# Kernel tuning notes

Measured on AMD Instinct MI355X. Metric: run time of the kernel, lower is better.

## Reference

```python
import jax, jax.numpy as jnp
import numpy as np

N = 50000   # nodes
E = 400000  # edges
H = 4       # heads
C = 64      # hidden per head
IN = 8
G = 64      # graphs in batch
NEG_SLOPE = 0.2


def setup_inputs() -> dict:
    key = jax.random.key(0)
    ks = jax.random.split(key, 32)
    def w(k, shape, fan_in):
        return jax.random.normal(k, shape, jnp.float32) * (1.0 / np.sqrt(fan_in))
    inp = {}
    inp['x'] = jax.random.normal(ks[0], (N, IN), jnp.float32)
    inp['edge_index'] = jax.random.randint(ks[1], (2, E), 0, N, jnp.int32)
    inp['edge_attr'] = jax.random.normal(ks[2], (E, 1), jnp.float32)
    inp['batch'] = jnp.sort(jax.random.randint(ks[3], (N,), 0, G, jnp.int32))
    # encoder
    inp['enc_w'] = w(ks[4], (IN, H * 16), IN)[:, :64]  # [8,64]
    inp['enc_b'] = jnp.zeros((64,), jnp.float32)
    # gat1: in 64 -> H*C = 256
    inp['g1_wl'] = w(ks[5], (64, H * C), 64)
    inp['g1_bl'] = jnp.zeros((H * C,), jnp.float32)
    inp['g1_wr'] = w(ks[6], (64, H * C), 64)
    inp['g1_we'] = w(ks[7], (1, H * C), 1)
    inp['g1_att'] = w(ks[8], (H, C), C)
    inp['g1_b'] = jnp.zeros((H * C,), jnp.float32)
    # gat2: in 256 -> H*C = 256
    inp['g2_wl'] = w(ks[9], (H * C, H * C), H * C)
    inp['g2_bl'] = jnp.zeros((H * C,), jnp.float32)
    inp['g2_wr'] = w(ks[10], (H * C, H * C), H * C)
    inp['g2_we'] = w(ks[11], (1, H * C), 1)
    inp['g2_att'] = w(ks[12], (H, C), C)
    inp['g2_b'] = jnp.zeros((H * C,), jnp.float32)
    # post MLP: 256 -> 128 -> LN -> ReLU -> 128 -> 64 -> ReLU
    inp['p1_w'] = w(ks[13], (H * C, 128), H * C)
    inp['p1_b'] = jnp.zeros((128,), jnp.float32)
    inp['ln_g'] = jnp.ones((128,), jnp.float32)
    inp['ln_b'] = jnp.zeros((128,), jnp.float32)
    inp['p2_w'] = w(ks[14], (128, 64), 128)
    inp['p2_b'] = jnp.zeros((64,), jnp.float32)
    inp['head_w'] = w(ks[15], (64, 1), 64)
    inp['head_b'] = jnp.zeros((1,), jnp.float32)
    return inp


def gatv2_conv(h, src, dst, ea, wl, bl, wr, we, att, b):
    # PyG GATv2Conv (concat=True): message from src j aggregated at dst i
    xl = (h @ wl + bl).reshape(N, H, C)   # lin_l(x_j), carries source messages
    xr = (h @ wr).reshape(N, H, C)        # lin_r(x_i)
    e = (ea @ we).reshape(E, H, C)        # lin_edge(edge_attr)
    s = jax.nn.leaky_relu(xl[src] + xr[dst] + e, NEG_SLOPE)  # [E,H,C]
    logits = jnp.einsum('ehc,hc->eh', s, att)                # [E,H]
    # softmax over incoming edges of each dst node
    mx = jax.ops.segment_max(logits, dst, num_segments=N)
    ex = jnp.exp(logits - mx[dst])
    denom = jax.ops.segment_sum(ex, dst, num_segments=N)
    alpha = ex / (denom[dst] + 1e-16)                        # [E,H]
    out = jax.ops.segment_sum(alpha[:, :, None] * xl[src], dst, num_segments=N)
    return out.reshape(N, H * C) + b


def reference(x, edge_index, edge_attr, batch, enc_w, enc_b,
              g1_wl, g1_bl, g1_wr, g1_we, g1_att, g1_b,
              g2_wl, g2_bl, g2_wr, g2_we, g2_att, g2_b,
              p1_w, p1_b, ln_g, ln_b, p2_w, p2_b, head_w, head_b):
    src, dst = edge_index[0], edge_index[1]
    h = jax.nn.relu(x @ enc_w + enc_b)
    h = jax.nn.relu(gatv2_conv(h, src, dst, edge_attr, g1_wl, g1_bl, g1_wr, g1_we, g1_att, g1_b))
    h = jax.nn.relu(gatv2_conv(h, src, dst, edge_attr, g2_wl, g2_bl, g2_wr, g2_we, g2_att, g2_b))
    # global mean pool per graph
    s = jax.ops.segment_sum(h, batch, num_segments=G)
    cnt = jax.ops.segment_sum(jnp.ones((N,), h.dtype), batch, num_segments=G)
    g = s / jnp.maximum(cnt, 1.0)[:, None]                   # [G, H*C]
    # post MLP (dropout is identity in eval)
    z = g @ p1_w + p1_b
    mu = jnp.mean(z, axis=-1, keepdims=True)
    var = jnp.mean((z - mu) ** 2, axis=-1, keepdims=True)
    z = (z - mu) * jax.lax.rsqrt(var + 1e-5) * ln_g + ln_b
    z = jax.nn.relu(z)
    z = jax.nn.relu(z @ p2_w + p2_b)
    return (z @ head_w + head_b).squeeze(-1)                 # [G]
```

## Files before the change

kernel.cpp:

```cpp
#include <hip/hip_runtime.h>
#include <hip/hip_bf16.h>
#include <math.h>

#define NN 50000
#define NE 400000
#define HH 4
#define CC 64
#define HC 256
#define GG 64
#define NB 196
#define ENCB 12500
#define WCB 640

typedef short v8s __attribute__((ext_vector_type(8)));
typedef float f32x4 __attribute__((ext_vector_type(4)));

static __device__ inline unsigned short f2bf(float v) {
  __hip_bfloat16 b = __float2bfloat16(v);
  return *reinterpret_cast<unsigned short*>(&b);
}
static __device__ inline float bflo(unsigned u) { return __uint_as_float(u << 16); }
static __device__ inline float bfhi(unsigned u) { return __uint_as_float(u & 0xffff0000u); }

static __device__ inline void gload_lds16(const void* g, void* l) {
  __builtin_amdgcn_global_load_lds(
      (const __attribute__((address_space(1))) void*)g,
      (__attribute__((address_space(3))) void*)l, 16, 0, 0);
}

__global__ __launch_bounds__(256) void head_kernel(
    const float* __restrict__ x, const float* __restrict__ enc_w,
    const float* __restrict__ enc_b, unsigned short* __restrict__ h0,
    const float* __restrict__ g1_wl, const float* __restrict__ g1_wr,
    const float* __restrict__ g2_wl, const float* __restrict__ g2_wr,
    unsigned short* __restrict__ wt1, unsigned short* __restrict__ wt2,
    const int* __restrict__ batch, int* __restrict__ deg,
    float* __restrict__ pool, int* __restrict__ bounds) {
  int bid = blockIdx.x, tid = threadIdx.x;
  if (bid < ENCB) {
    int idx = bid * 256 + tid;
    int node = idx >> 6, col = idx & 63;
    const float* xr = x + node * 8;
    float acc = enc_b[col];
#pragma unroll
    for (int k = 0; k < 8; ++k) acc += xr[k] * enc_w[k * 64 + col];
    h0[idx] = f2bf(fmaxf(acc, 0.f));
  } else if (bid < ENCB + WCB) {
    int idx = (bid - ENCB) * 256 + tid;
    const float* W; unsigned short* Wt; int K; int base;
    if (idx < 16384)        { W = g1_wl; Wt = wt1;                     K = 64;  base = idx; }
    else if (idx < 32768)   { W = g1_wr; Wt = wt1 + (size_t)256 * 64;  K = 64;  base = idx - 16384; }
    else if (idx < 98304)   { W = g2_wl; Wt = wt2;                     K = 256; base = idx - 32768; }
    else if (idx < 163840)  { W = g2_wr; Wt = wt2 + (size_t)256 * 256; K = 256; base = idx - 98304; }
    else return;
    int k = base >> 8, n = base & 255;
    Wt[n * K + k] = f2bf(W[base]);
  } else {
    int sb = bid - ENCB - WCB;
    int i = sb * 256 + tid;
    if (i < NN) deg[i] = 0;
    if (sb < GG) pool[sb * 256 + tid] = 0.f;
    if (sb == NB - 1 && tid <= GG) {
      int g = tid, lo = 0, hi = NN;
      while (lo < hi) {
        int mid = (lo + hi) >> 1;
        if (batch[mid] < g) lo = mid + 1; else hi = mid;
      }
      bounds[g] = lo;
    }
  }
}

template <int K, bool FILL>
__global__ __launch_bounds__(256) void matmul_mfma_kernel(
    const unsigned short* __restrict__ A, const unsigned short* __restrict__ Wt,
    const float* __restrict__ bias,
    unsigned short* __restrict__ outL, unsigned short* __restrict__ outR, int M,
    const int* __restrict__ ei, const float* __restrict__ ea,
    int* __restrict__ cursor, int2* __restrict__ edges) {
  const int mmb = ((M + 127) >> 7) << 2;
  int bid = blockIdx.x;
  if (FILL && bid >= mmb) {
    int e = (bid - mmb) * 256 + threadIdx.x;
    if (e < NE) {
      int d = ei[NE + e];
      int pos = atomicAdd(&cursor[d], 1);
      edges[pos] = make_int2(ei[e] << 9, __float_as_int(ea[e]));
    }
    return;
  }
  {
    int q = mmb >> 3, r = mmb & 7;
    int xcd = bid & 7, off2 = bid >> 3;
    bid = (xcd < r ? xcd * (q + 1) : r * (q + 1) + (xcd - r) * q) + off2;
  }
  __shared__ __attribute__((aligned(16))) unsigned short lds[8192];
  const int tid = threadIdx.x;
  const int wave = tid >> 6;
  const int lane = tid & 63;
  const int quad = lane >> 4;
  const int lrow = lane & 15;
  const int wr = (wave & 1) * 64;
  const int wc = (wave >> 1) * 64;
  const int r0 = (bid >> 2) * 128;
  const int n0 = (bid & 3) * 128;

  f32x4 acc[4][4];
#pragma unroll
  for (int i = 0; i < 4; ++i)
#pragma unroll
    for (int j = 0; j < 4; ++j) acc[i][j] = (f32x4){0.f, 0.f, 0.f, 0.f};

  const int lrA0 = (wave * 2) * 16 + (lane >> 2);
  const int lrA1 = lrA0 + 16;
  const int c    = lane & 3;
  const int cs0  = c ^ ((lrA0 >> 1) & 3);
  const int cs1  = c ^ ((lrA1 >> 1) & 3);
  int ga0 = r0 + lrA0; if (ga0 >= M) ga0 = M - 1;
  int ga1 = r0 + lrA1; if (ga1 >= M) ga1 = M - 1;
  const unsigned short* srcA0 = A  + (size_t)ga0 * K + cs0 * 8;
  const unsigned short* srcA1 = A  + (size_t)ga1 * K + cs1 * 8;
  const unsigned short* srcB0 = Wt + (size_t)(n0 + lrA0) * K + cs0 * 8;
  const unsigned short* srcB1 = Wt + (size_t)(n0 + lrA1) * K + cs1 * 8;
  unsigned short* dA0 = &lds[(wave * 2 + 0) * 512];
  unsigned short* dA1 = &lds[(wave * 2 + 1) * 512];
  unsigned short* dB0 = &lds[4096 + (wave * 2 + 0) * 512];
  unsigned short* dB1 = &lds[4096 + (wave * 2 + 1) * 512];
  const int qsw = (quad ^ ((lrow >> 1) & 3)) * 8;

  for (int k0 = 0; k0 < K; k0 += 32) {
    gload_lds16(srcA0 + k0, dA0);
    gload_lds16(srcA1 + k0, dA1);
    gload_lds16(srcB0 + k0, dB0);
    gload_lds16(srcB1 + k0, dB1);
    __syncthreads();

    v8s af[4], bf[4];
#pragma unroll
    for (int rt = 0; rt < 4; ++rt)
      af[rt] = *(const v8s*)&lds[(wr + rt * 16 + lrow) * 32 + qsw];
#pragma unroll
    for (int ct = 0; ct < 4; ++ct)
      bf[ct] = *(const v8s*)&lds[4096 + (wc + ct * 16 + lrow) * 32 + qsw];
#pragma unroll
    for (int rt = 0; rt < 4; ++rt)
#pragma unroll
      for (int ct = 0; ct < 4; ++ct)
        acc[rt][ct] = __builtin_amdgcn_mfma_f32_16x16x32_bf16(af[rt], bf[ct], acc[rt][ct], 0, 0, 0);
    __syncthreads();
  }

  const bool isL = (n0 < 256);
  unsigned short* outp = isL ? outL : outR;
  const int cbase = isL ? n0 : (n0 - 256);
  constexpr int SP = 136;
  unsigned short* stage = lds;

#pragma unroll
  for (int rt = 0; rt < 4; ++rt) {
    __syncthreads();
#pragma unroll
    for (int ct = 0; ct < 4; ++ct) {
      int col = wc + ct * 16 + lrow;
      float b = isL ? bias[cbase + col] : 0.f;
#pragma unroll
      for (int r = 0; r < 4; ++r) {
        int sr = (wave & 1) * 16 + quad * 4 + r;
        stage[sr * SP + col] = f2bf(acc[rt][ct][r] + b);
      }
    }
    __syncthreads();
    int sr = tid >> 3;
    int c0 = (tid & 7) * 16;
    int grow = r0 + (sr >> 4) * 64 + rt * 16 + (sr & 15);
    if (grow < M) {
      uint4 v0 = *(const uint4*)&stage[sr * SP + c0];
      uint4 v1 = *(const uint4*)&stage[sr * SP + c0 + 8];
      *(uint4*)&outp[(size_t)grow * 256 + cbase + c0] = v0;
      *(uint4*)&outp[(size_t)grow * 256 + cbase + c0 + 8] = v1;
    }
  }
}

__global__ void degree_kernel(const int* __restrict__ ei, int* __restrict__ deg) {
  int e = blockIdx.x * 256 + threadIdx.x;
  if (e < NE) atomicAdd(&deg[ei[NE + e]], 1);
}

__global__ __launch_bounds__(256) void blocksum_kernel(
    const int* __restrict__ deg, int* __restrict__ bsum) {
  int t = threadIdx.x;
  int i = blockIdx.x * 256 + t;
  int v = (i < NN) ? deg[i] : 0;
#pragma unroll
  for (int off = 32; off; off >>= 1) v += __shfl_down(v, off, 64);
  __shared__ int ws[4];
  if ((t & 63) == 0) ws[t >> 6] = v;
  __syncthreads();
  if (t == 0) bsum[blockIdx.x] = ws[0] + ws[1] + ws[2] + ws[3];
}

__global__ __launch_bounds__(256) void blockscan_kernel(
    const int* __restrict__ bsum, int* __restrict__ bpre, int* __restrict__ rowstart) {
  __shared__ int s[256];
  int t = threadIdx.x;
  int v = (t < NB) ? bsum[t] : 0;
  s[t] = v;
  __syncthreads();
  for (int off = 1; off < 256; off <<= 1) {
    int x = s[t];
    int y = (t >= off) ? s[t - off] : 0;
    __syncthreads();
    s[t] = x + y;
    __syncthreads();
  }
  if (t < NB) bpre[t] = s[t] - v;
  if (t == 255) rowstart[NN] = s[255];
}

__global__ __launch_bounds__(256) void rowstart_kernel(
    const int* __restrict__ deg, const int* __restrict__ bpre,
    int* __restrict__ rowstart, int* __restrict__ cursor) {
  __shared__ int s[256];
  int t = threadIdx.x;
  int i = blockIdx.x * 256 + t;
  int v = (i < NN) ? deg[i] : 0;
  s[t] = v;
  __syncthreads();
  for (int off = 1; off < 256; off <<= 1) {
    int x = s[t];
    int y = (t >= off) ? s[t - off] : 0;
    __syncthreads();
    s[t] = x + y;
    __syncthreads();
  }
  if (i < NN) {
    int rs = bpre[blockIdx.x] + s[t] - v;
    rowstart[i] = rs;
    cursor[i] = rs;
  }
}

__global__ __launch_bounds__(256) void gat_fused_kernel(
    const int* __restrict__ rowstart, const int2* __restrict__ edges,
    const unsigned short* __restrict__ xl, const unsigned short* __restrict__ xr,
    const float* __restrict__ we, const float* __restrict__ att,
    const float* __restrict__ bias, unsigned short* __restrict__ outb) {
  int node = (blockIdx.x * 256 + threadIdx.x) >> 6;
  int lane = threadIdx.x & 63;
  int r0 = __builtin_amdgcn_readfirstlane(rowstart[node]);
  int r1 = __builtin_amdgcn_readfirstlane(rowstart[node + 1]);
  const char* xlp = (const char*)xl + lane * 8;
  uint2 rp = ((const uint2*)xr)[(size_t)node * 64 + lane];
  float4 r = make_float4(bflo(rp.x), bfhi(rp.x), bflo(rp.y), bfhi(rp.y));
  float4 wv = ((const float4*)we)[lane];
  float4 at = ((const float4*)att)[lane];
  const float LOG2E = 1.442695040888963f;
  at.x *= LOG2E; at.y *= LOG2E; at.z *= LOG2E; at.w *= LOG2E;
  float4 acc = make_float4(0.f, 0.f, 0.f, 0.f);
  float denom = 0.f;

  auto edge_step = [&](float eav, uint2 p) {
    float4 a = make_float4(bflo(p.x), bfhi(p.x), bflo(p.y), bfhi(p.y));
    float s0 = a.x + (r.x + eav * wv.x);
    float s1 = a.y + (r.y + eav * wv.y);
    float s2 = a.z + (r.z + eav * wv.z);
    float s3 = a.w + (r.w + eav * wv.w);
    s0 = fmaxf(s0, 0.2f * s0);
    s1 = fmaxf(s1, 0.2f * s1);
    s2 = fmaxf(s2, 0.2f * s2);
    s3 = fmaxf(s3, 0.2f * s3);
    float p4 = (s0 * at.x + s1 * at.y) + (s2 * at.z + s3 * at.w);
#pragma unroll
    for (int off = 8; off; off >>= 1) p4 += __shfl_xor(p4, off, 16);
    float ex = exp2f(p4);
    denom += ex;
    acc.x += ex * a.x; acc.y += ex * a.y; acc.z += ex * a.z; acc.w += ex * a.w;
  };

  int i = r0;
  for (; i + 4 <= r1; i += 4) {
    int2 e0 = edges[i];     int2 e1 = edges[i + 1];
    int2 e2 = edges[i + 2]; int2 e3 = edges[i + 3];
    uint2 p0 = *(const uint2*)(xlp + (unsigned)e0.x);
    uint2 p1 = *(const uint2*)(xlp + (unsigned)e1.x);
    uint2 p2 = *(const uint2*)(xlp + (unsigned)e2.x);
    uint2 p3 = *(const uint2*)(xlp + (unsigned)e3.x);
    edge_step(__int_as_float(e0.y), p0);
    edge_step(__int_as_float(e1.y), p1);
    edge_step(__int_as_float(e2.y), p2);
    edge_step(__int_as_float(e3.y), p3);
  }
  for (; i < r1; ++i) {
    int2 e = edges[i];
    edge_step(__int_as_float(e.y), *(const uint2*)(xlp + (unsigned)e.x));
  }

  float inv = 1.f / (denom + 1e-16f);
  float4 bv = ((const float4*)bias)[lane];
  float4 o;
  o.x = fmaxf(acc.x * inv + bv.x, 0.f);
  o.y = fmaxf(acc.y * inv + bv.y, 0.f);
  o.z = fmaxf(acc.z * inv + bv.z, 0.f);
  o.w = fmaxf(acc.w * inv + bv.w, 0.f);
  uint2 pk;
  pk.x = (unsigned)f2bf(o.x) | ((unsigned)f2bf(o.y) << 16);
  pk.y = (unsigned)f2bf(o.z) | ((unsigned)f2bf(o.w) << 16);
  ((uint2*)outb)[(size_t)node * 64 + lane] = pk;
}

__global__ __launch_bounds__(256) void pool_kernel(
    const unsigned short* __restrict__ h, const int* __restrict__ batch,
    float* __restrict__ pool) {
  int rg = threadIdx.x >> 6;
  int lane = threadIdx.x & 63;
  int n0 = blockIdx.x * 64;
  const uint2* h2 = (const uint2*)h;
  float4 acc = make_float4(0.f, 0.f, 0.f, 0.f);
  int cur = -1;
#pragma unroll 4
  for (int i = 0; i < 16; ++i) {
    int n = n0 + rg + 4 * i;
    if (n >= NN) break;
    int b = batch[n];
    if (b != cur) {
      if (cur >= 0) {
        float* p = &pool[cur * 256 + lane * 4];
        atomicAdd(p + 0, acc.x); atomicAdd(p + 1, acc.y);
        atomicAdd(p + 2, acc.z); atomicAdd(p + 3, acc.w);
      }
      cur = b;
      acc = make_float4(0.f, 0.f, 0.f, 0.f);
    }
    uint2 v = h2[(size_t)n * 64 + lane];
    acc.x += bflo(v.x); acc.y += bfhi(v.x);
    acc.z += bflo(v.y); acc.w += bfhi(v.y);
  }
  if (cur >= 0) {
    float* p = &pool[cur * 256 + lane * 4];
    atomicAdd(p + 0, acc.x); atomicAdd(p + 1, acc.y);
    atomicAdd(p + 2, acc.z); atomicAdd(p + 3, acc.w);
  }
}

__global__ __launch_bounds__(128) void mlp_kernel(
    const float* __restrict__ pool, const int* __restrict__ bounds,
    const float* __restrict__ p1w, const float* __restrict__ p1b,
    const float* __restrict__ lng, const float* __restrict__ lnb,
    const float* __restrict__ p2w, const float* __restrict__ p2b,
    const float* __restrict__ hw, const float* __restrict__ hb,
    float* __restrict__ out) {
  __shared__ float sg[256];
  __shared__ float red[128];
  __shared__ float sz[128];
  __shared__ float s2[64];
  int b = blockIdx.x, tid = threadIdx.x;
  float cntf = (float)(bounds[b + 1] - bounds[b]);
  float invc = 1.f / fmaxf(cntf, 1.f);
  for (int i = tid; i < 256; i += 128) sg[i] = pool[b * 256 + i] * invc;
  __syncthreads();
  float z = p1b[tid];
  for (int k = 0; k < 256; ++k) z += sg[k] * p1w[k * 128 + tid];
  red[tid] = z; __syncthreads();
  for (int off = 64; off; off >>= 1) { if (tid < off) red[tid] += red[tid + off]; __syncthreads(); }
  float mu = red[0] * (1.f / 128.f);
  __syncthreads();
  float d = z - mu;
  red[tid] = d * d; __syncthreads();
  for (int off = 64; off; off >>= 1) { if (tid < off) red[tid] += red[tid + off]; __syncthreads(); }
  float var = red[0] * (1.f / 128.f);
  float zn = d * rsqrtf(var + 1e-5f) * lng[tid] + lnb[tid];
  sz[tid] = fmaxf(zn, 0.f);
  __syncthreads();
  if (tid < 64) {
    float a = p2b[tid];
    for (int k = 0; k < 128; ++k) a += sz[k] * p2w[k * 64 + tid];
    s2[tid] = fmaxf(a, 0.f);
  }
  __syncthreads();
  if (tid < 64) {
    float p = s2[tid] * hw[tid];
    for (int off = 32; off; off >>= 1) p += __shfl_down(p, off, 64);
    if (tid == 0) out[b] = p + hb[0];
  }
}

extern "C" void kernel_launch(void* const* d_in, const int* in_sizes, int n_in,
                              void* d_out, int out_size, void* d_ws, size_t ws_size,
                              hipStream_t stream) {
  const float* x      = (const float*)d_in[0];
  const int*   ei     = (const int*)d_in[1];
  const float* ea     = (const float*)d_in[2];
  const int*   batch  = (const int*)d_in[3];
  const float* enc_w  = (const float*)d_in[4];
  const float* enc_b  = (const float*)d_in[5];
  const float* g1_wl  = (const float*)d_in[6];
  const float* g1_bl  = (const float*)d_in[7];
  const float* g1_wr  = (const float*)d_in[8];
  const float* g1_we  = (const float*)d_in[9];
  const float* g1_att = (const float*)d_in[10];
  const float* g1_b   = (const float*)d_in[11];
  const float* g2_wl  = (const float*)d_in[12];
  const float* g2_bl  = (const float*)d_in[13];
  const float* g2_wr  = (const float*)d_in[14];
  const float* g2_we  = (const float*)d_in[15];
  const float* g2_att = (const float*)d_in[16];
  const float* g2_b   = (const float*)d_in[17];
  const float* p1_w   = (const float*)d_in[18];
  const float* p1_b   = (const float*)d_in[19];
  const float* ln_g   = (const float*)d_in[20];
  const float* ln_b   = (const float*)d_in[21];
  const float* p2_w   = (const float*)d_in[22];
  const float* p2_b   = (const float*)d_in[23];
  const float* head_w = (const float*)d_in[24];
  const float* head_b = (const float*)d_in[25];
  float* out = (float*)d_out;

  char* ws = (char*)d_ws;
  size_t off = 0;
  auto alloc = [&](size_t bytes) -> void* {
    void* p = ws + off;
    off = (off + bytes + 255) & ~(size_t)255;
    return p;
  };
  unsigned short* xl   = (unsigned short*)alloc((size_t)NN * HC * 2);
  unsigned short* xr   = (unsigned short*)alloc((size_t)NN * HC * 2);
  unsigned short* h0   = (unsigned short*)alloc((size_t)NN * 64 * 2);
  unsigned short* hb16 = (unsigned short*)alloc((size_t)NN * HC * 2);
  unsigned short* wt1  = (unsigned short*)alloc((size_t)512 * 64 * 2);
  unsigned short* wt2  = (unsigned short*)alloc((size_t)512 * 256 * 2);
  float* pool      = (float*)alloc((size_t)GG * HC * 4);
  int*   deg       = (int*)alloc((size_t)NN * 4);
  int*   rowstart  = (int*)alloc((size_t)(NN + 1) * 4);
  int*   cursor    = (int*)alloc((size_t)NN * 4);
  int*   bsum      = (int*)alloc((size_t)NB * 4);
  int*   bpre      = (int*)alloc((size_t)NB * 4);
  int2*  edges     = (int2*)alloc((size_t)NE * 8);
  int*   bounds    = (int*)alloc((size_t)(GG + 1) * 4);

  head_kernel<<<ENCB + WCB + NB, 256, 0, stream>>>(
      x, enc_w, enc_b, h0, g1_wl, g1_wr, g2_wl, g2_wr, wt1, wt2,
      batch, deg, pool, bounds);

  degree_kernel<<<(NE + 255) / 256, 256, 0, stream>>>(ei, deg);
  blocksum_kernel<<<NB, 256, 0, stream>>>(deg, bsum);
  blockscan_kernel<<<1, 256, 0, stream>>>(bsum, bpre, rowstart);
  rowstart_kernel<<<NB, 256, 0, stream>>>(deg, bpre, rowstart, cursor);

  const int MMB = ((NN + 127) / 128) * 4;
  const int FB  = (NE + 255) / 256;

  matmul_mfma_kernel<64, true><<<MMB + FB, 256, 0, stream>>>(
      h0, wt1, g1_bl, xl, xr, NN, ei, ea, cursor, edges);
  gat_fused_kernel<<<NN / 4, 256, 0, stream>>>(rowstart, edges, xl, xr,
                                               g1_we, g1_att, g1_b, hb16);

  matmul_mfma_kernel<256, false><<<MMB, 256, 0, stream>>>(
      hb16, wt2, g2_bl, xl, xr, NN, nullptr, nullptr, nullptr, nullptr);
  gat_fused_kernel<<<NN / 4, 256, 0, stream>>>(rowstart, edges, xl, xr,
                                               g2_we, g2_att, g2_b, hb16);

  pool_kernel<<<(NN + 63) / 64, 256, 0, stream>>>(hb16, batch, pool);
  mlp_kernel<<<GG, 128, 0, stream>>>(pool, bounds, p1_w, p1_b, ln_g, ln_b,
                                     p2_w, p2_b, head_w, head_b, out);
}
```

Baseline: 337.1 us.

## Double-buffer LDS in MFMA matmul and split edge fill into own kernel

The matmul K-loop now uses two LDS buffers, issuing the next tile's global-to-LDS loads before computing on the current tile, which removes one barrier per iteration and overlaps loads with MFMA work. The CSR edge-fill blocks that were folded into the first matmul launch move into a separate fill_kernel launched beforehand. LDS per block doubles, which may reduce occupancy, and the split adds a kernel launch while giving up the overlap between fill and the first matmul.

```diff
diff --git a/kernel.cpp b/kernel.cpp
--- a/kernel.cpp
+++ b/kernel.cpp
@@ -71,30 +71,19 @@
   }
 }
 
-template <int K, bool FILL>
+template <int K>
 __global__ __launch_bounds__(256) void matmul_mfma_kernel(
     const unsigned short* __restrict__ A, const unsigned short* __restrict__ Wt,
     const float* __restrict__ bias,
-    unsigned short* __restrict__ outL, unsigned short* __restrict__ outR, int M,
-    const int* __restrict__ ei, const float* __restrict__ ea,
-    int* __restrict__ cursor, int2* __restrict__ edges) {
+    unsigned short* __restrict__ outL, unsigned short* __restrict__ outR, int M) {
   const int mmb = ((M + 127) >> 7) << 2;
   int bid = blockIdx.x;
-  if (FILL && bid >= mmb) {
-    int e = (bid - mmb) * 256 + threadIdx.x;
-    if (e < NE) {
-      int d = ei[NE + e];
-      int pos = atomicAdd(&cursor[d], 1);
-      edges[pos] = make_int2(ei[e] << 9, __float_as_int(ea[e]));
-    }
-    return;
-  }
   {
     int q = mmb >> 3, r = mmb & 7;
     int xcd = bid & 7, off2 = bid >> 3;
     bid = (xcd < r ? xcd * (q + 1) : r * (q + 1) + (xcd - r) * q) + off2;
   }
-  __shared__ __attribute__((aligned(16))) unsigned short lds[8192];
+  __shared__ __attribute__((aligned(16))) unsigned short lds[16384];
   const int tid = threadIdx.x;
   const int wave = tid >> 6;
   const int lane = tid & 63;
@@ -122,32 +111,43 @@
   const unsigned short* srcA1 = A  + (size_t)ga1 * K + cs1 * 8;
   const unsigned short* srcB0 = Wt + (size_t)(n0 + lrA0) * K + cs0 * 8;
   const unsigned short* srcB1 = Wt + (size_t)(n0 + lrA1) * K + cs1 * 8;
-  unsigned short* dA0 = &lds[(wave * 2 + 0) * 512];
-  unsigned short* dA1 = &lds[(wave * 2 + 1) * 512];
-  unsigned short* dB0 = &lds[4096 + (wave * 2 + 0) * 512];
-  unsigned short* dB1 = &lds[4096 + (wave * 2 + 1) * 512];
+  const int doff0 = (wave * 2 + 0) * 512;
+  const int doff1 = (wave * 2 + 1) * 512;
   const int qsw = (quad ^ ((lrow >> 1) & 3)) * 8;
 
-  for (int k0 = 0; k0 < K; k0 += 32) {
-    gload_lds16(srcA0 + k0, dA0);
-    gload_lds16(srcA1 + k0, dA1);
-    gload_lds16(srcB0 + k0, dB0);
-    gload_lds16(srcB1 + k0, dB1);
-    __syncthreads();
-
+  constexpr int NT = K / 32;
+  gload_lds16(srcA0, &lds[doff0]);
+  gload_lds16(srcA1, &lds[doff1]);
+  gload_lds16(srcB0, &lds[4096 + doff0]);
+  gload_lds16(srcB1, &lds[4096 + doff1]);
+  __syncthreads();
+
+  int cur = 0;
+#pragma unroll
+  for (int t = 0; t < NT; ++t) {
+    if (t + 1 < NT) {
+      const int k0 = (t + 1) * 32;
+      const int nb = (cur ^ 1) * 8192;
+      gload_lds16(srcA0 + k0, &lds[nb + doff0]);
+      gload_lds16(srcA1 + k0, &lds[nb + doff1]);
+      gload_lds16(srcB0 + k0, &lds[nb + 4096 + doff0]);
+      gload_lds16(srcB1 + k0, &lds[nb + 4096 + doff1]);
+    }
+    const unsigned short* base = &lds[cur * 8192];
     v8s af[4], bf[4];
 #pragma unroll
     for (int rt = 0; rt < 4; ++rt)
-      af[rt] = *(const v8s*)&lds[(wr + rt * 16 + lrow) * 32 + qsw];
+      af[rt] = *(const v8s*)&base[(wr + rt * 16 + lrow) * 32 + qsw];
 #pragma unroll
     for (int ct = 0; ct < 4; ++ct)
-      bf[ct] = *(const v8s*)&lds[4096 + (wc + ct * 16 + lrow) * 32 + qsw];
+      bf[ct] = *(const v8s*)&base[4096 + (wc + ct * 16 + lrow) * 32 + qsw];
 #pragma unroll
     for (int rt = 0; rt < 4; ++rt)
 #pragma unroll
       for (int ct = 0; ct < 4; ++ct)
         acc[rt][ct] = __builtin_amdgcn_mfma_f32_16x16x32_bf16(af[rt], bf[ct], acc[rt][ct], 0, 0, 0);
     __syncthreads();
+    cur ^= 1;
   }
 
   const bool isL = (n0 < 256);
@@ -238,6 +238,16 @@
     int rs = bpre[blockIdx.x] + s[t] - v;
     rowstart[i] = rs;
     cursor[i] = rs;
+  }
+}
+
+__global__ void fill_kernel(const int* __restrict__ ei, const float* __restrict__ ea,
+                            int* __restrict__ cursor, int2* __restrict__ edges) {
+  int e = blockIdx.x * 256 + threadIdx.x;
+  if (e < NE) {
+    int d = ei[NE + e];
+    int pos = atomicAdd(&cursor[d], 1);
+    edges[pos] = make_int2(ei[e] << 9, __float_as_int(ea[e]));
   }
 }
 
@@ -446,17 +456,15 @@
   blocksum_kernel<<<NB, 256, 0, stream>>>(deg, bsum);
   blockscan_kernel<<<1, 256, 0, stream>>>(bsum, bpre, rowstart);
   rowstart_kernel<<<NB, 256, 0, stream>>>(deg, bpre, rowstart, cursor);
+  fill_kernel<<<(NE + 255) / 256, 256, 0, stream>>>(ei, ea, cursor, edges);
 
   const int MMB = ((NN + 127) / 128) * 4;
-  const int FB  = (NE + 255) / 256;
-
-  matmul_mfma_kernel<64, true><<<MMB + FB, 256, 0, stream>>>(
-      h0, wt1, g1_bl, xl, xr, NN, ei, ea, cursor, edges);
+
+  matmul_mfma_kernel<64><<<MMB, 256, 0, stream>>>(h0, wt1, g1_bl, xl, xr, NN);
   gat_fused_kernel<<<NN / 4, 256, 0, stream>>>(rowstart, edges, xl, xr,
                                                g1_we, g1_att, g1_b, hb16);
 
-  matmul_mfma_kernel<256, false><<<MMB, 256, 0, stream>>>(
-      hb16, wt2, g2_bl, xl, xr, NN, nullptr, nullptr, nullptr, nullptr);
+  matmul_mfma_kernel<256><<<MMB, 256, 0, stream>>>(hb16, wt2, g2_bl, xl, xr, NN);
   gat_fused_kernel<<<NN / 4, 256, 0, stream>>>(rowstart, edges, xl, xr,
                                                g2_we, g2_att, g2_b, hb16);
 
```

Measured after the change: 327.9 us. -2.7%, faster.
